# Kernel optimization log

Hardware: AMD Instinct MI355X
Metric: run time of the kernel (lower is better)

Reference implementation:

```python
import jax, jax.numpy as jnp
import numpy as np
import math

B, T, Z, H, DOF = 256, 200, 64, 256, 12
NUM_LINKS = 13
POS_DIM = (NUM_LINKS + 1) * 3  # 42
TIME_BANDS = 6
TIME_DIM = 2 * TIME_BANDS + 1  # 13
ACTION_SCALE = 0.25
TRACK_ALPHA = 1.0
SIGMA_MIN, SIGMA_MAX = 0.05, 0.5


def setup_inputs() -> dict:
    key = jax.random.key(0)
    ks = iter(jax.random.split(key, 32))
    rn = lambda shape, s=0.1: jax.random.normal(next(ks), shape, jnp.float32) * s
    inp = {
        'z': jax.random.normal(next(ks), (B, Z), jnp.float32),
        'W_hz': rn((H, Z)), 'b_hz': rn((H,)),
        'W_cz': rn((H, Z)), 'b_cz': rn((H,)),
        'Wih': rn((4 * H, DOF + Z + TIME_DIM)), 'Whh': rn((4 * H, H)),
        'bih': rn((4 * H,)), 'bhh': rn((4 * H,)),
        'Wp1': rn((H, H)), 'bp1': rn((H,)),
        'Wp2': rn((DOF, H)), 'bp2': rn((DOF,)),
        'Wo1': rn((H, H)), 'bo1': rn((H,)),
        'Wo2': rn((3, H)), 'bo2': rn((3,)),
        'Wv': rn((POS_DIM, H)), 'bv': rn((POS_DIM,)),
        'Wfk': rn((NUM_LINKS * 3, DOF)), 'bfk': rn((NUM_LINKS * 3,)),
        'pos_mean': jax.random.normal(next(ks), (NUM_LINKS + 1, 3), jnp.float32),
        'pos_std': 0.5 + jax.random.uniform(next(ks), (NUM_LINKS + 1, 3), jnp.float32),
        'joint_lower': -jnp.ones((DOF,), jnp.float32),
        'joint_upper': jnp.ones((DOF,), jnp.float32),
        'default_dof_pos': jnp.zeros((DOF,), jnp.float32),
    }
    return inp


def _time_features():
    t = jnp.linspace(0.0, 1.0, T)
    feats = [t]
    for k in range(TIME_BANDS):
        f = 2.0 ** k
        feats.append(jnp.sin(2 * math.pi * f * t))
        feats.append(jnp.cos(2 * math.pi * f * t))
    return jnp.stack(feats, axis=-1)  # [T, TIME_DIM]


def reference(z, W_hz, b_hz, W_cz, b_cz, Wih, Whh, bih, bhh,
              Wp1, bp1, Wp2, bp2, Wo1, bo1, Wo2, bo2, Wv, bv, Wfk, bfk,
              pos_mean, pos_std, joint_lower, joint_upper, default_dof_pos):
    joint_range = (joint_upper - joint_lower) / 2.0
    joint_mean = (joint_upper + joint_lower) / 2.0
    time_feats = _time_features()  # [T, TIME_DIM]

    h0 = z @ W_hz.T + b_hz  # [B,H]
    c0 = z @ W_cz.T + b_cz
    prev0 = jnp.broadcast_to(default_dof_pos, (B, DOF))

    def step(carry, tf):
        h, c, prev = carry
        prev_norm = (prev - joint_mean) / joint_range
        x = jnp.concatenate([prev_norm, z, jnp.broadcast_to(tf, (B, TIME_DIM))], axis=-1)
        g = x @ Wih.T + bih + h @ Whh.T + bhh  # [B,4H]
        i, f, gg, o = jnp.split(g, 4, axis=-1)
        c_new = jax.nn.sigmoid(f) * c + jax.nn.sigmoid(i) * jnp.tanh(gg)
        h_new = jax.nn.sigmoid(o) * jnp.tanh(c_new)
        action = jnp.tanh(jax.nn.relu(h_new @ Wp1.T + bp1) @ Wp2.T + bp2)
        target = action * ACTION_SCALE + default_dof_pos
        cur = prev + TRACK_ALPHA * (target - prev)
        clamped = jnp.clip(cur, joint_lower, joint_upper)
        cur_in = cur + jax.lax.stop_gradient(clamped - cur)  # straight-through clamp
        obj = jax.nn.relu(h_new @ Wo1.T + bo1) @ Wo2.T + bo2
        return (h_new, c_new, jax.lax.stop_gradient(cur_in)), (h_new, action, cur, obj)

    _, (H_seq, actions, joints, objs) = jax.lax.scan(step, (h0, c0, prev0), time_feats)
    # [T,B,*] -> [B,T,*]
    H_seq = jnp.swapaxes(H_seq, 0, 1)
    actions_seq = jnp.swapaxes(actions, 0, 1)
    joint_traj = jnp.swapaxes(joints, 0, 1)
    object_traj = jnp.swapaxes(objs, 0, 1)

    agent_traj = joint_traj @ Wfk.T + bfk  # FK: [B,T,39]
    combined = jnp.concatenate([agent_traj, object_traj], axis=-1)  # [B,T,42]
    combined_rs = combined.reshape(B, T, NUM_LINKS + 1, 3)
    graph_x_mu = ((combined_rs - pos_mean) / pos_std).reshape(B, T, POS_DIM)

    sigma = SIGMA_MIN + (SIGMA_MAX - SIGMA_MIN) * jax.nn.sigmoid(H_seq @ Wv.T + bv)
    log_sigma_pos = jnp.log(sigma)
    return (graph_x_mu, joint_traj, actions_seq, log_sigma_pos)
```

## Files before the change

### kernel.cpp

```cpp
#include <hip/hip_runtime.h>
#include <math.h>

#define B_ 256
#define T_ 200
#define H_ 256
#define DOF_ 12

typedef __bf16 bf16;
typedef __bf16 bf16x8 __attribute__((ext_vector_type(8)));
typedef float f32x4 __attribute__((ext_vector_type(4)));
typedef unsigned long long u64;

#define XK 288
#define XPAD 296
#define P1PAD 264

#define PI_D 3.14159265358979323846

#define OFF_TF     0u
#define OFF_TCONP  10400u
#define OFF_ZCP    829600u
#define OFF_H0     1878176u
#define OFF_C0     2140320u
#define OFF_WCOMB  2402464u
#define OFF_WP1    2992288u
#define OFF_WP2    3123360u
#define OFF_WO1    3131552u
#define OFF_WO2    3262624u
#define OFF_WV     3270816u
#define OFF_HX     3295392u
#define OFF_HSEQ   3819680u

__device__ __forceinline__ float sigf(float x) { return 1.f / (1.f + __expf(-x)); }
__device__ __forceinline__ float tanh_f(float x) {
  float a = fabsf(x);
  float e = __expf(-2.f * a);
  float t = (1.f - e) / (1.f + e);
  return x < 0.f ? -t : t;
}

#define LBAR() asm volatile("s_waitcnt lgkmcnt(0)\n\ts_barrier" ::: "memory")

__global__ void k_tfeat(float* tf) {
  int i = blockIdx.x * blockDim.x + threadIdx.x;
  if (i >= T_ * 13) return;
  int t = i / 13, j = i % 13;
  float tv = (float)t / 199.f;
  float v;
  if (j == 0) v = tv;
  else {
    int k = (j - 1) >> 1;
    float f = (float)(1 << k);
    double arg = 2.0 * PI_D * (double)f * (double)tv;
    v = (j & 1) ? (float)sin(arg) : (float)cos(arg);
  }
  tf[i] = v;
}

__global__ void k_prep(const float* __restrict__ tf, const float* __restrict__ Wih,
                       const float* __restrict__ z,
                       const float* __restrict__ bih, const float* __restrict__ bhh,
                       const float* __restrict__ Whz, const float* __restrict__ bhz,
                       const float* __restrict__ Wcz, const float* __restrict__ bcz,
                       float* tconp, float* zcp, float* h0, float* c0) {
  int i = blockIdx.x * blockDim.x + threadIdx.x;
  if (i < 204800) {
    int g = i & 3, q = i >> 2;
    int m = q & 127, hm = (q >> 7) & 1, t = q >> 8;
    int n = g * 256 + 128 * hm + m;
    float s = 0.f;
    #pragma unroll
    for (int j = 0; j < 13; ++j) s += tf[t * 13 + j] * Wih[n * 89 + 76 + j];
    tconp[i] = s;
    return;
  }
  i -= 204800;
  if (i < 262144) {
    int r = i & 3, g = (i >> 2) & 3, tid = (i >> 4) & 511;
    int half = (i >> 13) & 1, pairk = i >> 14;
    int wv = tid >> 6, lr = tid & 15, lq = (tid >> 4) & 3;
    int b = pairk * 16 + lq * 4 + r;
    int n = g * 256 + 128 * half + 16 * wv + lr;
    float s = bih[n] + bhh[n];
    for (int k = 0; k < 64; ++k) s += z[b * 64 + k] * Wih[n * 89 + 12 + k];
    zcp[i] = s;
    return;
  }
  i -= 262144;
  if (i < 65536) {
    int b = i / 256, u = i % 256;
    float s = bhz[u];
    for (int k = 0; k < 64; ++k) s += z[b * 64 + k] * Whz[u * 64 + k];
    h0[i] = s;
    return;
  }
  i -= 65536;
  if (i < 65536) {
    int b = i / 256, u = i % 256;
    float s = bcz[u];
    for (int k = 0; k < 64; ++k) s += z[b * 64 + k] * Wcz[u * 64 + k];
    c0[i] = s;
  }
}

__global__ void k_cast(const float* __restrict__ Whh, const float* __restrict__ Wih,
                       const float* __restrict__ Wp1, const float* __restrict__ Wp2,
                       const float* __restrict__ Wo1, const float* __restrict__ Wo2,
                       const float* __restrict__ Wv,
                       bf16* Wcomb, bf16* Wp1b, bf16* Wp2b, bf16* Wo1b,
                       bf16* Wo2b, bf16* Wvb) {
  int i = blockIdx.x * blockDim.x + threadIdx.x;
  if (i < 294912) {
    int n = i / XK, k = i % XK;
    float v = (k < 256) ? Whh[n * 256 + k]
            : ((k < 268) ? Wih[n * 89 + (k - 256)] : 0.f);
    Wcomb[i] = (bf16)v;
    return;
  }
  i -= 294912;
  if (i < 65536) { Wp1b[i] = (bf16)Wp1[i]; return; }
  i -= 65536;
  if (i < 4096) { int r = i / 256; Wp2b[i] = (bf16)((r < 12) ? Wp2[i] : 0.f); return; }
  i -= 4096;
  if (i < 65536) { Wo1b[i] = (bf16)Wo1[i]; return; }
  i -= 65536;
  if (i < 4096) { int r = i / 256; Wo2b[i] = (bf16)((r < 3) ? Wo2[i] : 0.f); return; }
  i -= 4096;
  if (i < 12288) { int r = i / 256; Wvb[i] = (bf16)((r < 42) ? Wv[i] : 0.f); }
}

__global__ __launch_bounds__(512, 2) void k_recur(
    const float* __restrict__ zcp, const float* __restrict__ tconp,
    const float* __restrict__ h0, const float* __restrict__ c0,
    const bf16* __restrict__ Wcomb, const bf16* __restrict__ Wp1b,
    const bf16* __restrict__ Wp2b,
    const float* __restrict__ bp1, const float* __restrict__ bp2,
    const float* __restrict__ jlo, const float* __restrict__ jhi,
    const float* __restrict__ ddp,
    u64* hxt,
    bf16* __restrict__ Hseq, float* __restrict__ outJ, float* __restrict__ outA) {
  __shared__ bf16 xbuf[16][XPAD];
  __shared__ bf16 w1[272][P1PAD];
  __shared__ bf16 p1buf[16][P1PAD];
  const int tid = threadIdx.x;
  const int wv = tid >> 6, ln = tid & 63, lr = ln & 15, lq = ln >> 4;
  const int bid = blockIdx.x;
  const int pairk = ((bid >> 4) << 3) | (bid & 7);
  const int half = (bid >> 3) & 1;
  const int lbid = pairk * 2 + half;
  const int b0 = pairk * 16;
  const int u_loc = 16 * wv + lr;
  const int u_gl = 128 * half + u_loc;

  for (int i = tid; i < 272 * 32; i += 512) {
    int r = i >> 5, c8 = (i & 31) * 8;
    bf16x8 v = (r < 256)
      ? *reinterpret_cast<const bf16x8*>(&Wp1b[r * 256 + c8])
      : *reinterpret_cast<const bf16x8*>(&Wp2b[(r - 256) * 256 + c8]);
    *reinterpret_cast<bf16x8*>(&w1[r][c8]) = v;
  }
  for (int i = tid; i < 16 * XPAD; i += 512) {
    int r = i / XPAD, c = i % XPAD;
    float v = 0.f;
    if (c < 256) v = h0[(b0 + r) * 256 + c];
    else if (c < 268) {
      int d = c - 256;
      float lo = jlo[d], hi = jhi[d];
      v = (ddp[d] - 0.5f * (hi + lo)) / (0.5f * (hi - lo));
    }
    xbuf[r][c] = (bf16)v;
  }

  f32x4 wc0[9], wc1[9], wc2[9], wc3[9];
  #pragma unroll
  for (int kt = 0; kt < 9; ++kt) {
    wc0[kt] = *reinterpret_cast<const f32x4*>(&Wcomb[(size_t)(0 * 256 + u_gl) * XK + kt * 32 + lq * 8]);
    wc1[kt] = *reinterpret_cast<const f32x4*>(&Wcomb[(size_t)(1 * 256 + u_gl) * XK + kt * 32 + lq * 8]);
    wc2[kt] = *reinterpret_cast<const f32x4*>(&Wcomb[(size_t)(2 * 256 + u_gl) * XK + kt * 32 + lq * 8]);
    wc3[kt] = *reinterpret_cast<const f32x4*>(&Wcomb[(size_t)(3 * 256 + u_gl) * XK + kt * 32 + lq * 8]);
    asm volatile("" : "+a"(wc0[kt]), "+a"(wc1[kt]), "+a"(wc2[kt]), "+a"(wc3[kt]));
  }

  float c_reg[4];
  #pragma unroll
  for (int r = 0; r < 4; ++r) c_reg[r] = c0[(b0 + lq * 4 + r) * 256 + u_gl];
  f32x4 zcreg[4];
  #pragma unroll
  for (int g = 0; g < 4; ++g)
    zcreg[g] = *reinterpret_cast<const f32x4*>(
        zcp + ((size_t)lbid * 512 + tid) * 16 + g * 4);
  const float* tcb = tconp + (size_t)(half * 512 + u_loc * 4);
  const float bp1r0 = bp1[32 * wv + lr];
  const float bp1r1 = bp1[32 * wv + 16 + lr];
  float bp2r = 0.f, ddr = 0.f, lor = -1.f, hir = 1.f;
  if (lr < 12) { bp2r = bp2[lr]; ddr = ddp[lr]; lor = jlo[lr]; hir = jhi[lr]; }
  const float jmr = 0.5f * (hir + lor), jrr = 0.5f * (hir - lor);
  bf16* hs = Hseq + ((size_t)(b0 + lq * 4) * T_) * 256 + u_gl;

  const int wru = 16 * wv + (ln >> 2), wrc = ln & 3;
  const int rcol = 128 * (half ^ 1) + wru;
  u64* pws0 = hxt + ((((size_t)(pairk * 2 + 0) * 2 + half) * 128 + u_loc) * 4 + lq) * 2;
  u64* pws1 = hxt + ((((size_t)(pairk * 2 + 1) * 2 + half) * 128 + u_loc) * 4 + lq) * 2;
  u64* prs0 = hxt + ((((size_t)(pairk * 2 + 0) * 2 + (half ^ 1)) * 128 + wru) * 4 + wrc) * 2;
  u64* prs1 = hxt + ((((size_t)(pairk * 2 + 1) * 2 + (half ^ 1)) * 128 + wru) * 4 + wrc) * 2;

  f32x4 tcv = *reinterpret_cast<const f32x4*>(tcb);
  __syncthreads();
  bool dead = false;

  for (int t = 0; t < T_; ++t) {
    f32x4 ac[4];
    #pragma unroll
    for (int g = 0; g < 4; ++g) ac[g] = zcreg[g] + tcv[g];
    #pragma unroll
    for (int kt = 0; kt < 9; ++kt) {
      bf16x8 a = *reinterpret_cast<const bf16x8*>(&xbuf[lr][kt * 32 + lq * 8]);
      asm volatile("" : "+a"(wc0[kt]), "+a"(wc1[kt]), "+a"(wc2[kt]), "+a"(wc3[kt]));
      ac[0] = __builtin_amdgcn_mfma_f32_16x16x32_bf16(a, __builtin_bit_cast(bf16x8, wc0[kt]), ac[0], 0, 0, 0);
      ac[1] = __builtin_amdgcn_mfma_f32_16x16x32_bf16(a, __builtin_bit_cast(bf16x8, wc1[kt]), ac[1], 0, 0, 0);
      ac[2] = __builtin_amdgcn_mfma_f32_16x16x32_bf16(a, __builtin_bit_cast(bf16x8, wc2[kt]), ac[2], 0, 0, 0);
      ac[3] = __builtin_amdgcn_mfma_f32_16x16x32_bf16(a, __builtin_bit_cast(bf16x8, wc3[kt]), ac[3], 0, 0, 0);
    }
    LBAR();

    union { u64 v[1]; unsigned short s[4]; } pk;
    bf16 hb4[4];
    #pragma unroll
    for (int r = 0; r < 4; ++r) {
      float cn = sigf(ac[1][r]) * c_reg[r] + sigf(ac[0][r]) * tanh_f(ac[2][r]);
      float hn = sigf(ac[3][r]) * tanh_f(cn);
      c_reg[r] = cn;
      bf16 hb = (bf16)hn;
      hb4[r] = hb;
      pk.s[r] = __builtin_bit_cast(unsigned short, hb);
    }
    const unsigned int want = t + 1;
    {
      u64 q0 = ((u64)want << 32) | (u64)pk.s[0] | ((u64)pk.s[1] << 16);
      u64 q1 = ((u64)want << 32) | (u64)pk.s[2] | ((u64)pk.s[3] << 16);
      u64* pw = (t & 1) ? pws1 : pws0;
      __hip_atomic_store(pw, q0, __ATOMIC_RELAXED, __HIP_MEMORY_SCOPE_AGENT);
      __hip_atomic_store(pw + 1, q1, __ATOMIC_RELAXED, __HIP_MEMORY_SCOPE_AGENT);
    }
    #pragma unroll
    for (int r = 0; r < 4; ++r) {
      xbuf[lq * 4 + r][u_gl] = hb4[r];
      hs[(size_t)r * (T_ * 256) + (size_t)t * 256] = hb4[r];
    }
    f32x4 tcn = *reinterpret_cast<const f32x4*>(
        tcb + (size_t)((t + 1 < T_) ? t + 1 : t) * 1024);

    u64 pq0, pq1;
    {
      u64* pr = (t & 1) ? prs1 : prs0;
      int guard = 1 << 16;
      for (;;) {
        pq0 = __hip_atomic_load(pr, __ATOMIC_RELAXED, __HIP_MEMORY_SCOPE_AGENT);
        pq1 = __hip_atomic_load(pr + 1, __ATOMIC_RELAXED, __HIP_MEMORY_SCOPE_AGENT);
        int ok = ((unsigned)(pq0 >> 32) == want) & ((unsigned)(pq1 >> 32) == want);
        if (__all(ok)) break;
        if (dead || --guard == 0) { dead = true; break; }
      }
    }
    xbuf[wrc * 4 + 0][rcol] = __builtin_bit_cast(bf16, (unsigned short)(pq0));
    xbuf[wrc * 4 + 1][rcol] = __builtin_bit_cast(bf16, (unsigned short)(pq0 >> 16));
    xbuf[wrc * 4 + 2][rcol] = __builtin_bit_cast(bf16, (unsigned short)(pq1));
    xbuf[wrc * 4 + 3][rcol] = __builtin_bit_cast(bf16, (unsigned short)(pq1 >> 16));
    LBAR();

    {
      f32x4 acc0 = {bp1r0, bp1r0, bp1r0, bp1r0};
      f32x4 acc1 = {bp1r1, bp1r1, bp1r1, bp1r1};
      #pragma unroll
      for (int kt = 0; kt < 8; ++kt) {
        bf16x8 av = *reinterpret_cast<const bf16x8*>(&xbuf[lr][kt * 32 + lq * 8]);
        bf16x8 b0v = *reinterpret_cast<const bf16x8*>(&w1[32 * wv + lr][kt * 32 + lq * 8]);
        bf16x8 b1v = *reinterpret_cast<const bf16x8*>(&w1[32 * wv + 16 + lr][kt * 32 + lq * 8]);
        acc0 = __builtin_amdgcn_mfma_f32_16x16x32_bf16(av, b0v, acc0, 0, 0, 0);
        acc1 = __builtin_amdgcn_mfma_f32_16x16x32_bf16(av, b1v, acc1, 0, 0, 0);
      }
      #pragma unroll
      for (int r = 0; r < 4; ++r) {
        p1buf[lq * 4 + r][32 * wv + lr] = (bf16)fmaxf(acc0[r], 0.f);
        p1buf[lq * 4 + r][32 * wv + 16 + lr] = (bf16)fmaxf(acc1[r], 0.f);
      }
    }
    LBAR();

    if (wv == 0) {
      f32x4 acc = {0.f, 0.f, 0.f, 0.f};
      #pragma unroll
      for (int kt = 0; kt < 8; ++kt) {
        bf16x8 ap = *reinterpret_cast<const bf16x8*>(&p1buf[lr][kt * 32 + lq * 8]);
        bf16x8 w2 = *reinterpret_cast<const bf16x8*>(&w1[256 + lr][kt * 32 + lq * 8]);
        acc = __builtin_amdgcn_mfma_f32_16x16x32_bf16(ap, w2, acc, 0, 0, 0);
      }
      if (lr < 12) {
        #pragma unroll
        for (int r = 0; r < 4; ++r) {
          int b = lq * 4 + r;
          float act = tanh_f(acc[r] + bp2r);
          float curp = act * 0.25f + ddr;
          float cl = fminf(fmaxf(curp, lor), hir);
          if (half == 0) {
            size_t o = ((size_t)(b0 + b) * T_ + t) * 12 + lr;
            outA[o] = act;
            outJ[o] = curp;
          }
          xbuf[b][256 + lr] = (bf16)((cl - jmr) / jrr);
        }
      }
    }
    LBAR();
    tcv = tcn;
  }
}

__global__ __launch_bounds__(256) void k_post(
    const bf16* __restrict__ Hseq, const bf16* __restrict__ Wo1b,
    const bf16* __restrict__ Wo2b, const bf16* __restrict__ Wvb,
    const float* __restrict__ bo1, const float* __restrict__ bo2,
    const float* __restrict__ bv,
    const float* __restrict__ Wfk, const float* __restrict__ bfk,
    const float* __restrict__ pm, const float* __restrict__ ps,
    const float* __restrict__ joints, float* __restrict__ out0,
    float* __restrict__ out3) {
  __shared__ bf16 u1buf[16][P1PAD];
  __shared__ float objbuf[16][3];
  __shared__ float jbuf[16][12];
  const int tid = threadIdx.x;
  const int wv = tid >> 6;
  const int ln = tid & 63;
  const int lr = ln & 15;
  const int lq = ln >> 4;

  bf16x8 wo1f[4][8];
  float bo1r[4];
  #pragma unroll
  for (int jn = 0; jn < 4; ++jn) {
    int n0 = wv * 64 + jn * 16;
    bo1r[jn] = bo1[n0 + lr];
    #pragma unroll
    for (int kt = 0; kt < 8; ++kt)
      wo1f[jn][kt] = *reinterpret_cast<const bf16x8*>(
          &Wo1b[(size_t)(n0 + lr) * 256 + kt * 32 + lq * 8]);
  }
  const int col = (wv - 1) * 16 + lr;
  bf16x8 wvf[8];
  float bvr = 0.f;
  if (wv >= 1) {
    #pragma unroll
    for (int kt = 0; kt < 8; ++kt)
      wvf[kt] = *reinterpret_cast<const bf16x8*>(
          &Wvb[(size_t)col * 256 + kt * 32 + lq * 8]);
    bvr = (col < 42) ? bv[col] : 0.f;
  }
  bf16x8 wo2f[8];
  if (wv == 0) {
    #pragma unroll
    for (int kt = 0; kt < 8; ++kt)
      wo2f[kt] = *reinterpret_cast<const bf16x8*>(
          &Wo2b[(size_t)lr * 256 + kt * 32 + lq * 8]);
  }

  for (int it = 0; it < 10; ++it) {
    int tt = blockIdx.x * 10 + it;
    size_t r0 = (size_t)tt * 16;
    bf16x8 ah[8];
    #pragma unroll
    for (int kt = 0; kt < 8; ++kt)
      ah[kt] = *reinterpret_cast<const bf16x8*>(&Hseq[(r0 + lr) * 256 + kt * 32 + lq * 8]);
    #pragma unroll
    for (int jn = 0; jn < 4; ++jn) {
      int n0 = wv * 64 + jn * 16;
      float bb = bo1r[jn];
      f32x4 acc = {bb, bb, bb, bb};
      #pragma unroll
      for (int kt = 0; kt < 8; ++kt)
        acc = __builtin_amdgcn_mfma_f32_16x16x32_bf16(ah[kt], wo1f[jn][kt], acc, 0, 0, 0);
      #pragma unroll
      for (int r = 0; r < 4; ++r)
        u1buf[lq * 4 + r][n0 + lr] = (bf16)fmaxf(acc[r], 0.f);
    }
    if (wv >= 1) {
      f32x4 acc = {bvr, bvr, bvr, bvr};
      #pragma unroll
      for (int kt = 0; kt < 8; ++kt)
        acc = __builtin_amdgcn_mfma_f32_16x16x32_bf16(ah[kt], wvf[kt], acc, 0, 0, 0);
      if (col < 42) {
        #pragma unroll
        for (int r = 0; r < 4; ++r) {
          float s = 0.05f + 0.45f * sigf(acc[r]);
          out3[(r0 + lq * 4 + r) * 42 + col] = __logf(s);
        }
      }
    }
    if (tid < 192) {
      int rr = tid / 12, d = tid % 12;
      jbuf[rr][d] = joints[(r0 + rr) * 12 + d];
    }
    __syncthreads();
    if (wv == 0) {
      bf16x8 ap[8];
      #pragma unroll
      for (int kt = 0; kt < 8; ++kt)
        ap[kt] = *reinterpret_cast<const bf16x8*>(&u1buf[lr][kt * 32 + lq * 8]);
      f32x4 acc = {0.f, 0.f, 0.f, 0.f};
      #pragma unroll
      for (int kt = 0; kt < 8; ++kt)
        acc = __builtin_amdgcn_mfma_f32_16x16x32_bf16(ap[kt], wo2f[kt], acc, 0, 0, 0);
      if (lr < 3) {
        #pragma unroll
        for (int r = 0; r < 4; ++r)
          objbuf[lq * 4 + r][lr] = acc[r] + bo2[lr];
      }
    }
    __syncthreads();
    for (int e = tid; e < 16 * 42; e += 256) {
      int rr = e / 42, pd = e % 42;
      float v;
      if (pd < 39) {
        float s = bfk[pd];
        #pragma unroll
        for (int d = 0; d < 12; ++d) s += jbuf[rr][d] * Wfk[pd * 12 + d];
        v = s;
      } else v = objbuf[rr][pd - 39];
      out0[(r0 + rr) * 42 + pd] = (v - pm[pd]) / ps[pd];
    }
    __syncthreads();
  }
}

extern "C" void kernel_launch(void* const* d_in, const int* in_sizes, int n_in,
                              void* d_out, int out_size, void* d_ws, size_t ws_size,
                              hipStream_t stream) {
  const float* z   = (const float*)d_in[0];
  const float* Whz = (const float*)d_in[1];
  const float* bhz = (const float*)d_in[2];
  const float* Wcz = (const float*)d_in[3];
  const float* bcz = (const float*)d_in[4];
  const float* Wih = (const float*)d_in[5];
  const float* Whh = (const float*)d_in[6];
  const float* bih = (const float*)d_in[7];
  const float* bhh = (const float*)d_in[8];
  const float* Wp1 = (const float*)d_in[9];
  const float* bp1 = (const float*)d_in[10];
  const float* Wp2 = (const float*)d_in[11];
  const float* bp2 = (const float*)d_in[12];
  const float* Wo1 = (const float*)d_in[13];
  const float* bo1 = (const float*)d_in[14];
  const float* Wo2 = (const float*)d_in[15];
  const float* bo2 = (const float*)d_in[16];
  const float* Wv  = (const float*)d_in[17];
  const float* bv  = (const float*)d_in[18];
  const float* Wfk = (const float*)d_in[19];
  const float* bfk = (const float*)d_in[20];
  const float* pm  = (const float*)d_in[21];
  const float* ps  = (const float*)d_in[22];
  const float* jlo = (const float*)d_in[23];
  const float* jhi = (const float*)d_in[24];
  const float* ddp = (const float*)d_in[25];

  char* ws = (char*)d_ws;
  float* tf    = (float*)(ws + OFF_TF);
  float* tconp = (float*)(ws + OFF_TCONP);
  float* zcp   = (float*)(ws + OFF_ZCP);
  float* h0    = (float*)(ws + OFF_H0);
  float* c0    = (float*)(ws + OFF_C0);
  bf16* Wcomb  = (bf16*)(ws + OFF_WCOMB);
  bf16* Wp1b   = (bf16*)(ws + OFF_WP1);
  bf16* Wp2b   = (bf16*)(ws + OFF_WP2);
  bf16* Wo1b   = (bf16*)(ws + OFF_WO1);
  bf16* Wo2b   = (bf16*)(ws + OFF_WO2);
  bf16* Wvb    = (bf16*)(ws + OFF_WV);
  u64* hxt     = (u64*)(ws + OFF_HX);
  bf16* Hseq   = (bf16*)(ws + OFF_HSEQ);

  float* out  = (float*)d_out;
  float* out0 = out;
  float* outJ = out + 2150400;
  float* outA = out + 2764800;
  float* out3 = out + 3379200;

  k_tfeat<<<11, 256, 0, stream>>>(tf);
  k_prep<<<2336, 256, 0, stream>>>(tf, Wih, z, bih, bhh, Whz, bhz, Wcz, bcz,
                                   tconp, zcp, h0, c0);
  k_cast<<<1744, 256, 0, stream>>>(Whh, Wih, Wp1, Wp2, Wo1, Wo2, Wv,
                                   Wcomb, Wp1b, Wp2b, Wo1b, Wo2b, Wvb);
  k_recur<<<32, 512, 0, stream>>>(zcp, tconp, h0, c0, Wcomb, Wp1b, Wp2b,
                                  bp1, bp2, jlo, jhi, ddp, hxt,
                                  Hseq, outJ, outA);
  k_post<<<320, 256, 0, stream>>>(Hseq, Wo1b, Wo2b, Wvb, bo1, bo2, bv,
                                  Wfk, bfk, pm, ps, outJ, out0, out3);
}
```

Measured before the change: 1.119 ms.

## Halve recurrent kernel block size, giving each wave two hidden-unit tiles

The recurrent LSTM kernel now runs 256 threads (4 waves) per block instead of 512, and each wave computes two 16-unit slices of the gate GEMM, keeping twice as many weight fragments in accumulation registers. The cross-block hidden-state exchange reads four packed words per lane instead of two, and the Wp1 stage issues four MFMAs per k-step per wave. The intent is cheaper per-step barriers and more MFMA work per wave on the serial critical path, at the cost of register pressure (72 AGPR vectors) and less latency hiding. tanh also uses a hardware reciprocal instead of a divide.

```diff
diff --git a/kernel.cpp b/kernel.cpp
--- a/kernel.cpp
+++ b/kernel.cpp
@@ -35,7 +35,7 @@
 __device__ __forceinline__ float tanh_f(float x) {
   float a = fabsf(x);
   float e = __expf(-2.f * a);
-  float t = (1.f - e) / (1.f + e);
+  float t = (1.f - e) * __builtin_amdgcn_rcpf(1.f + e);
   return x < 0.f ? -t : t;
 }
 
@@ -129,7 +129,7 @@
   if (i < 12288) { int r = i / 256; Wvb[i] = (bf16)((r < 42) ? Wv[i] : 0.f); }
 }
 
-__global__ __launch_bounds__(512, 2) void k_recur(
+__global__ __launch_bounds__(256, 1) void k_recur(
     const float* __restrict__ zcp, const float* __restrict__ tconp,
     const float* __restrict__ h0, const float* __restrict__ c0,
     const bf16* __restrict__ Wcomb, const bf16* __restrict__ Wp1b,
@@ -149,17 +149,15 @@
   const int half = (bid >> 3) & 1;
   const int lbid = pairk * 2 + half;
   const int b0 = pairk * 16;
-  const int u_loc = 16 * wv + lr;
-  const int u_gl = 128 * half + u_loc;
-
-  for (int i = tid; i < 272 * 32; i += 512) {
+
+  for (int i = tid; i < 272 * 32; i += 256) {
     int r = i >> 5, c8 = (i & 31) * 8;
     bf16x8 v = (r < 256)
       ? *reinterpret_cast<const bf16x8*>(&Wp1b[r * 256 + c8])
       : *reinterpret_cast<const bf16x8*>(&Wp2b[(r - 256) * 256 + c8]);
     *reinterpret_cast<bf16x8*>(&w1[r][c8]) = v;
   }
-  for (int i = tid; i < 16 * XPAD; i += 512) {
+  for (int i = tid; i < 16 * XPAD; i += 256) {
     int r = i / XPAD, c = i % XPAD;
     float v = 0.f;
     if (c < 256) v = h0[(b0 + r) * 256 + c];
@@ -171,118 +169,173 @@
     xbuf[r][c] = (bf16)v;
   }
 
-  f32x4 wc0[9], wc1[9], wc2[9], wc3[9];
-  #pragma unroll
-  for (int kt = 0; kt < 9; ++kt) {
-    wc0[kt] = *reinterpret_cast<const f32x4*>(&Wcomb[(size_t)(0 * 256 + u_gl) * XK + kt * 32 + lq * 8]);
-    wc1[kt] = *reinterpret_cast<const f32x4*>(&Wcomb[(size_t)(1 * 256 + u_gl) * XK + kt * 32 + lq * 8]);
-    wc2[kt] = *reinterpret_cast<const f32x4*>(&Wcomb[(size_t)(2 * 256 + u_gl) * XK + kt * 32 + lq * 8]);
-    wc3[kt] = *reinterpret_cast<const f32x4*>(&Wcomb[(size_t)(3 * 256 + u_gl) * XK + kt * 32 + lq * 8]);
-    asm volatile("" : "+a"(wc0[kt]), "+a"(wc1[kt]), "+a"(wc2[kt]), "+a"(wc3[kt]));
-  }
-
-  float c_reg[4];
-  #pragma unroll
-  for (int r = 0; r < 4; ++r) c_reg[r] = c0[(b0 + lq * 4 + r) * 256 + u_gl];
-  f32x4 zcreg[4];
-  #pragma unroll
-  for (int g = 0; g < 4; ++g)
-    zcreg[g] = *reinterpret_cast<const f32x4*>(
-        zcp + ((size_t)lbid * 512 + tid) * 16 + g * 4);
-  const float* tcb = tconp + (size_t)(half * 512 + u_loc * 4);
-  const float bp1r0 = bp1[32 * wv + lr];
-  const float bp1r1 = bp1[32 * wv + 16 + lr];
+  f32x4 wc[2][4][9];
+  #pragma unroll
+  for (int ji = 0; ji < 2; ++ji) {
+    const int ug = 128 * half + 32 * wv + 16 * ji + lr;
+    #pragma unroll
+    for (int g = 0; g < 4; ++g)
+      #pragma unroll
+      for (int kt = 0; kt < 9; ++kt)
+        wc[ji][g][kt] = *reinterpret_cast<const f32x4*>(
+            &Wcomb[(size_t)(g * 256 + ug) * XK + kt * 32 + lq * 8]);
+  }
+  #pragma unroll
+  for (int kt = 0; kt < 9; ++kt)
+    asm volatile("" : "+a"(wc[0][0][kt]), "+a"(wc[0][1][kt]),
+                      "+a"(wc[0][2][kt]), "+a"(wc[0][3][kt]),
+                      "+a"(wc[1][0][kt]), "+a"(wc[1][1][kt]),
+                      "+a"(wc[1][2][kt]), "+a"(wc[1][3][kt]));
+
+  float c_reg[2][4];
+  f32x4 zcreg[2][4];
+  bf16* hs[2];
+  #pragma unroll
+  for (int ji = 0; ji < 2; ++ji) {
+    const int ug = 128 * half + 32 * wv + 16 * ji + lr;
+    #pragma unroll
+    for (int r = 0; r < 4; ++r) c_reg[ji][r] = c0[(b0 + lq * 4 + r) * 256 + ug];
+    const int tid512 = (2 * wv + ji) * 64 + ln;
+    #pragma unroll
+    for (int g = 0; g < 4; ++g)
+      zcreg[ji][g] = *reinterpret_cast<const f32x4*>(
+          zcp + ((size_t)lbid * 512 + tid512) * 16 + g * 4);
+    hs[ji] = Hseq + ((size_t)(b0 + lq * 4) * T_) * 256 + ug;
+  }
+  const float* tcb0 = tconp + (size_t)(half * 512 + (32 * wv + lr) * 4);
+  const float* tcb1 = tcb0 + 64;
+  float bp1r[4];
+  #pragma unroll
+  for (int jn = 0; jn < 4; ++jn) bp1r[jn] = bp1[64 * wv + 16 * jn + lr];
   float bp2r = 0.f, ddr = 0.f, lor = -1.f, hir = 1.f;
   if (lr < 12) { bp2r = bp2[lr]; ddr = ddp[lr]; lor = jlo[lr]; hir = jhi[lr]; }
   const float jmr = 0.5f * (hir + lor), jrr = 0.5f * (hir - lor);
-  bf16* hs = Hseq + ((size_t)(b0 + lq * 4) * T_) * 256 + u_gl;
-
-  const int wru = 16 * wv + (ln >> 2), wrc = ln & 3;
-  const int rcol = 128 * (half ^ 1) + wru;
-  u64* pws0 = hxt + ((((size_t)(pairk * 2 + 0) * 2 + half) * 128 + u_loc) * 4 + lq) * 2;
-  u64* pws1 = hxt + ((((size_t)(pairk * 2 + 1) * 2 + half) * 128 + u_loc) * 4 + lq) * 2;
-  u64* prs0 = hxt + ((((size_t)(pairk * 2 + 0) * 2 + (half ^ 1)) * 128 + wru) * 4 + wrc) * 2;
-  u64* prs1 = hxt + ((((size_t)(pairk * 2 + 1) * 2 + (half ^ 1)) * 128 + wru) * 4 + wrc) * 2;
-
-  f32x4 tcv = *reinterpret_cast<const f32x4*>(tcb);
+
+  u64* pws[2][2];
+  #pragma unroll
+  for (int ji = 0; ji < 2; ++ji) {
+    const int ul = 32 * wv + 16 * ji + lr;
+    #pragma unroll
+    for (int s = 0; s < 2; ++s)
+      pws[ji][s] = hxt + ((((size_t)(pairk * 2 + s) * 2 + half) * 128 + ul) * 4 + lq) * 2;
+  }
+  const int ru = 32 * wv + (ln >> 1);
+  const int rcol = 128 * (half ^ 1) + ru;
+  const int row0 = (ln & 1) * 8;
+  u64* prs[2];
+  #pragma unroll
+  for (int s = 0; s < 2; ++s)
+    prs[s] = hxt + ((((size_t)(pairk * 2 + s) * 2 + (half ^ 1)) * 128 + ru) * 4 + 2 * (ln & 1)) * 2;
+
+  f32x4 tcv0 = *reinterpret_cast<const f32x4*>(tcb0);
+  f32x4 tcv1 = *reinterpret_cast<const f32x4*>(tcb1);
   __syncthreads();
   bool dead = false;
 
   for (int t = 0; t < T_; ++t) {
-    f32x4 ac[4];
-    #pragma unroll
-    for (int g = 0; g < 4; ++g) ac[g] = zcreg[g] + tcv[g];
+    f32x4 ac[2][4];
+    #pragma unroll
+    for (int g = 0; g < 4; ++g) { ac[0][g] = zcreg[0][g] + tcv0[g]; ac[1][g] = zcreg[1][g] + tcv1[g]; }
     #pragma unroll
     for (int kt = 0; kt < 9; ++kt) {
       bf16x8 a = *reinterpret_cast<const bf16x8*>(&xbuf[lr][kt * 32 + lq * 8]);
-      asm volatile("" : "+a"(wc0[kt]), "+a"(wc1[kt]), "+a"(wc2[kt]), "+a"(wc3[kt]));
-      ac[0] = __builtin_amdgcn_mfma_f32_16x16x32_bf16(a, __builtin_bit_cast(bf16x8, wc0[kt]), ac[0], 0, 0, 0);
-      ac[1] = __builtin_amdgcn_mfma_f32_16x16x32_bf16(a, __builtin_bit_cast(bf16x8, wc1[kt]), ac[1], 0, 0, 0);
-      ac[2] = __builtin_amdgcn_mfma_f32_16x16x32_bf16(a, __builtin_bit_cast(bf16x8, wc2[kt]), ac[2], 0, 0, 0);
-      ac[3] = __builtin_amdgcn_mfma_f32_16x16x32_bf16(a, __builtin_bit_cast(bf16x8, wc3[kt]), ac[3], 0, 0, 0);
+      asm volatile("" : "+a"(wc[0][0][kt]), "+a"(wc[0][1][kt]),
+                        "+a"(wc[0][2][kt]), "+a"(wc[0][3][kt]),
+                        "+a"(wc[1][0][kt]), "+a"(wc[1][1][kt]),
+                        "+a"(wc[1][2][kt]), "+a"(wc[1][3][kt]));
+      #pragma unroll
+      for (int ji = 0; ji < 2; ++ji)
+        #pragma unroll
+        for (int g = 0; g < 4; ++g)
+          ac[ji][g] = __builtin_amdgcn_mfma_f32_16x16x32_bf16(
+              a, __builtin_bit_cast(bf16x8, wc[ji][g][kt]), ac[ji][g], 0, 0, 0);
     }
     LBAR();
 
-    union { u64 v[1]; unsigned short s[4]; } pk;
-    bf16 hb4[4];
-    #pragma unroll
-    for (int r = 0; r < 4; ++r) {
-      float cn = sigf(ac[1][r]) * c_reg[r] + sigf(ac[0][r]) * tanh_f(ac[2][r]);
-      float hn = sigf(ac[3][r]) * tanh_f(cn);
-      c_reg[r] = cn;
-      bf16 hb = (bf16)hn;
-      hb4[r] = hb;
-      pk.s[r] = __builtin_bit_cast(unsigned short, hb);
-    }
     const unsigned int want = t + 1;
-    {
-      u64 q0 = ((u64)want << 32) | (u64)pk.s[0] | ((u64)pk.s[1] << 16);
-      u64 q1 = ((u64)want << 32) | (u64)pk.s[2] | ((u64)pk.s[3] << 16);
-      u64* pw = (t & 1) ? pws1 : pws0;
+    bf16 hb[2][4];
+    #pragma unroll
+    for (int ji = 0; ji < 2; ++ji) {
+      unsigned short s4[4];
+      #pragma unroll
+      for (int r = 0; r < 4; ++r) {
+        float cn = sigf(ac[ji][1][r]) * c_reg[ji][r] + sigf(ac[ji][0][r]) * tanh_f(ac[ji][2][r]);
+        float hn = sigf(ac[ji][3][r]) * tanh_f(cn);
+        c_reg[ji][r] = cn;
+        bf16 h = (bf16)hn;
+        hb[ji][r] = h;
+        s4[r] = __builtin_bit_cast(unsigned short, h);
+      }
+      u64 q0 = ((u64)want << 32) | (u64)s4[0] | ((u64)s4[1] << 16);
+      u64 q1 = ((u64)want << 32) | (u64)s4[2] | ((u64)s4[3] << 16);
+      u64* pw = pws[ji][t & 1];
       __hip_atomic_store(pw, q0, __ATOMIC_RELAXED, __HIP_MEMORY_SCOPE_AGENT);
       __hip_atomic_store(pw + 1, q1, __ATOMIC_RELAXED, __HIP_MEMORY_SCOPE_AGENT);
     }
     #pragma unroll
-    for (int r = 0; r < 4; ++r) {
-      xbuf[lq * 4 + r][u_gl] = hb4[r];
-      hs[(size_t)r * (T_ * 256) + (size_t)t * 256] = hb4[r];
-    }
-    f32x4 tcn = *reinterpret_cast<const f32x4*>(
-        tcb + (size_t)((t + 1 < T_) ? t + 1 : t) * 1024);
-
-    u64 pq0, pq1;
+    for (int ji = 0; ji < 2; ++ji) {
+      const int ug = 128 * half + 32 * wv + 16 * ji + lr;
+      #pragma unroll
+      for (int r = 0; r < 4; ++r) {
+        xbuf[lq * 4 + r][ug] = hb[ji][r];
+        hs[ji][(size_t)r * (T_ * 256) + (size_t)t * 256] = hb[ji][r];
+      }
+    }
     {
-      u64* pr = (t & 1) ? prs1 : prs0;
+      size_t tp = (size_t)((t + 1 < T_) ? t + 1 : t) * 1024;
+      f32x4 tn0 = *reinterpret_cast<const f32x4*>(tcb0 + tp);
+      f32x4 tn1 = *reinterpret_cast<const f32x4*>(tcb1 + tp);
+      tcv0 = tn0; tcv1 = tn1;
+    }
+
+    u64 pq0, pq1, pq2, pq3;
+    {
+      u64* pr = prs[t & 1];
       int guard = 1 << 16;
       for (;;) {
-        pq0 = __hip_atomic_load(pr, __ATOMIC_RELAXED, __HIP_MEMORY_SCOPE_AGENT);
+        pq0 = __hip_atomic_load(pr + 0, __ATOMIC_RELAXED, __HIP_MEMORY_SCOPE_AGENT);
         pq1 = __hip_atomic_load(pr + 1, __ATOMIC_RELAXED, __HIP_MEMORY_SCOPE_AGENT);
-        int ok = ((unsigned)(pq0 >> 32) == want) & ((unsigned)(pq1 >> 32) == want);
+        pq2 = __hip_atomic_load(pr + 2, __ATOMIC_RELAXED, __HIP_MEMORY_SCOPE_AGENT);
+        pq3 = __hip_atomic_load(pr + 3, __ATOMIC_RELAXED, __HIP_MEMORY_SCOPE_AGENT);
+        int ok = ((unsigned)(pq0 >> 32) == want) & ((unsigned)(pq1 >> 32) == want) &
+                 ((unsigned)(pq2 >> 32) == want) & ((unsigned)(pq3 >> 32) == want);
         if (__all(ok)) break;
         if (dead || --guard == 0) { dead = true; break; }
       }
     }
-    xbuf[wrc * 4 + 0][rcol] = __builtin_bit_cast(bf16, (unsigned short)(pq0));
-    xbuf[wrc * 4 + 1][rcol] = __builtin_bit_cast(bf16, (unsigned short)(pq0 >> 16));
-    xbuf[wrc * 4 + 2][rcol] = __builtin_bit_cast(bf16, (unsigned short)(pq1));
-    xbuf[wrc * 4 + 3][rcol] = __builtin_bit_cast(bf16, (unsigned short)(pq1 >> 16));
+    xbuf[row0 + 0][rcol] = __builtin_bit_cast(bf16, (unsigned short)(pq0));
+    xbuf[row0 + 1][rcol] = __builtin_bit_cast(bf16, (unsigned short)(pq0 >> 16));
+    xbuf[row0 + 2][rcol] = __builtin_bit_cast(bf16, (unsigned short)(pq1));
+    xbuf[row0 + 3][rcol] = __builtin_bit_cast(bf16, (unsigned short)(pq1 >> 16));
+    xbuf[row0 + 4][rcol] = __builtin_bit_cast(bf16, (unsigned short)(pq2));
+    xbuf[row0 + 5][rcol] = __builtin_bit_cast(bf16, (unsigned short)(pq2 >> 16));
+    xbuf[row0 + 6][rcol] = __builtin_bit_cast(bf16, (unsigned short)(pq3));
+    xbuf[row0 + 7][rcol] = __builtin_bit_cast(bf16, (unsigned short)(pq3 >> 16));
     LBAR();
 
     {
-      f32x4 acc0 = {bp1r0, bp1r0, bp1r0, bp1r0};
-      f32x4 acc1 = {bp1r1, bp1r1, bp1r1, bp1r1};
+      f32x4 pa0 = {bp1r[0], bp1r[0], bp1r[0], bp1r[0]};
+      f32x4 pa1 = {bp1r[1], bp1r[1], bp1r[1], bp1r[1]};
+      f32x4 pa2 = {bp1r[2], bp1r[2], bp1r[2], bp1r[2]};
+      f32x4 pa3 = {bp1r[3], bp1r[3], bp1r[3], bp1r[3]};
       #pragma unroll
       for (int kt = 0; kt < 8; ++kt) {
         bf16x8 av = *reinterpret_cast<const bf16x8*>(&xbuf[lr][kt * 32 + lq * 8]);
-        bf16x8 b0v = *reinterpret_cast<const bf16x8*>(&w1[32 * wv + lr][kt * 32 + lq * 8]);
-        bf16x8 b1v = *reinterpret_cast<const bf16x8*>(&w1[32 * wv + 16 + lr][kt * 32 + lq * 8]);
-        acc0 = __builtin_amdgcn_mfma_f32_16x16x32_bf16(av, b0v, acc0, 0, 0, 0);
-        acc1 = __builtin_amdgcn_mfma_f32_16x16x32_bf16(av, b1v, acc1, 0, 0, 0);
+        bf16x8 b0v = *reinterpret_cast<const bf16x8*>(&w1[64 * wv + lr][kt * 32 + lq * 8]);
+        bf16x8 b1v = *reinterpret_cast<const bf16x8*>(&w1[64 * wv + 16 + lr][kt * 32 + lq * 8]);
+        bf16x8 b2v = *reinterpret_cast<const bf16x8*>(&w1[64 * wv + 32 + lr][kt * 32 + lq * 8]);
+        bf16x8 b3v = *reinterpret_cast<const bf16x8*>(&w1[64 * wv + 48 + lr][kt * 32 + lq * 8]);
+        pa0 = __builtin_amdgcn_mfma_f32_16x16x32_bf16(av, b0v, pa0, 0, 0, 0);
+        pa1 = __builtin_amdgcn_mfma_f32_16x16x32_bf16(av, b1v, pa1, 0, 0, 0);
+        pa2 = __builtin_amdgcn_mfma_f32_16x16x32_bf16(av, b2v, pa2, 0, 0, 0);
+        pa3 = __builtin_amdgcn_mfma_f32_16x16x32_bf16(av, b3v, pa3, 0, 0, 0);
       }
       #pragma unroll
       for (int r = 0; r < 4; ++r) {
-        p1buf[lq * 4 + r][32 * wv + lr] = (bf16)fmaxf(acc0[r], 0.f);
-        p1buf[lq * 4 + r][32 * wv + 16 + lr] = (bf16)fmaxf(acc1[r], 0.f);
+        p1buf[lq * 4 + r][64 * wv + lr]      = (bf16)fmaxf(pa0[r], 0.f);
+        p1buf[lq * 4 + r][64 * wv + 16 + lr] = (bf16)fmaxf(pa1[r], 0.f);
+        p1buf[lq * 4 + r][64 * wv + 32 + lr] = (bf16)fmaxf(pa2[r], 0.f);
+        p1buf[lq * 4 + r][64 * wv + 48 + lr] = (bf16)fmaxf(pa3[r], 0.f);
       }
     }
     LBAR();
@@ -312,7 +365,6 @@
       }
     }
     LBAR();
-    tcv = tcn;
   }
 }
 
@@ -487,7 +539,7 @@
                                    tconp, zcp, h0, c0);
   k_cast<<<1744, 256, 0, stream>>>(Whh, Wih, Wp1, Wp2, Wo1, Wo2, Wv,
                                    Wcomb, Wp1b, Wp2b, Wo1b, Wo2b, Wvb);
-  k_recur<<<32, 512, 0, stream>>>(zcp, tconp, h0, c0, Wcomb, Wp1b, Wp2b,
+  k_recur<<<32, 256, 0, stream>>>(zcp, tconp, h0, c0, Wcomb, Wp1b, Wp2b,
                                   bp1, bp2, jlo, jhi, ddp, hxt,
                                   Hseq, outJ, outA);
   k_post<<<320, 256, 0, stream>>>(Hseq, Wo1b, Wo2b, Wvb, bo1, bo2, bv,
```

Measured after the change: 1.102 ms. About the same (-1.5%).

## Split LSTM recurrence hidden units across four blocks per batch group

Applied to the files above, without the earlier changes.

The recurrent kernel now splits each 16-row batch group's hidden units over four 256-thread blocks instead of two 512-thread blocks. That gives 64 blocks, each exchanging h slices with three peers through flag-tagged global atomics. Each wave now does a quarter of the hidden units, and the zc and time-bias terms are loaded from global memory every step instead of being held in registers. The aim is more parallelism across CUs on the serial time loop, at the cost of more cross-block polling traffic and sync latency per step; tanh division is also replaced by a hardware reciprocal.

```diff
diff --git a/kernel.cpp b/kernel.cpp
--- a/kernel.cpp
+++ b/kernel.cpp
@@ -35,7 +35,7 @@
 __device__ __forceinline__ float tanh_f(float x) {
   float a = fabsf(x);
   float e = __expf(-2.f * a);
-  float t = (1.f - e) / (1.f + e);
+  float t = (1.f - e) * __builtin_amdgcn_rcpf(1.f + e);
   return x < 0.f ? -t : t;
 }
 
@@ -65,9 +65,8 @@
                        float* tconp, float* zcp, float* h0, float* c0) {
   int i = blockIdx.x * blockDim.x + threadIdx.x;
   if (i < 204800) {
-    int g = i & 3, q = i >> 2;
-    int m = q & 127, hm = (q >> 7) & 1, t = q >> 8;
-    int n = g * 256 + 128 * hm + m;
+    int g = i & 3, u = (i >> 2) & 255, t = i >> 10;
+    int n = g * 256 + u;
     float s = 0.f;
     #pragma unroll
     for (int j = 0; j < 13; ++j) s += tf[t * 13 + j] * Wih[n * 89 + 76 + j];
@@ -76,11 +75,11 @@
   }
   i -= 204800;
   if (i < 262144) {
-    int r = i & 3, g = (i >> 2) & 3, tid = (i >> 4) & 511;
-    int half = (i >> 13) & 1, pairk = i >> 14;
-    int wv = tid >> 6, lr = tid & 15, lq = (tid >> 4) & 3;
-    int b = pairk * 16 + lq * 4 + r;
-    int n = g * 256 + 128 * half + 16 * wv + lr;
+    int r = i & 3, g = (i >> 2) & 3, tid = (i >> 4) & 255, bid = i >> 12;
+    int quarter = bid >> 4, grp = bid & 15;
+    int wv = tid >> 6, ln = tid & 63, lr = ln & 15, lq = (ln >> 4) & 3;
+    int b = grp * 16 + lq * 4 + r;
+    int n = g * 256 + 64 * quarter + 16 * wv + lr;
     float s = bih[n] + bhh[n];
     for (int k = 0; k < 64; ++k) s += z[b * 64 + k] * Wih[n * 89 + 12 + k];
     zcp[i] = s;
@@ -129,7 +128,7 @@
   if (i < 12288) { int r = i / 256; Wvb[i] = (bf16)((r < 42) ? Wv[i] : 0.f); }
 }
 
-__global__ __launch_bounds__(512, 2) void k_recur(
+__global__ __launch_bounds__(256, 1) void k_recur(
     const float* __restrict__ zcp, const float* __restrict__ tconp,
     const float* __restrict__ h0, const float* __restrict__ c0,
     const bf16* __restrict__ Wcomb, const bf16* __restrict__ Wp1b,
@@ -145,21 +144,18 @@
   const int tid = threadIdx.x;
   const int wv = tid >> 6, ln = tid & 63, lr = ln & 15, lq = ln >> 4;
   const int bid = blockIdx.x;
-  const int pairk = ((bid >> 4) << 3) | (bid & 7);
-  const int half = (bid >> 3) & 1;
-  const int lbid = pairk * 2 + half;
-  const int b0 = pairk * 16;
-  const int u_loc = 16 * wv + lr;
-  const int u_gl = 128 * half + u_loc;
-
-  for (int i = tid; i < 272 * 32; i += 512) {
+  const int quarter = bid >> 4, grp = bid & 15;
+  const int b0 = grp * 16;
+  const int u_gl = 64 * quarter + 16 * wv + lr;
+
+  for (int i = tid; i < 272 * 32; i += 256) {
     int r = i >> 5, c8 = (i & 31) * 8;
     bf16x8 v = (r < 256)
       ? *reinterpret_cast<const bf16x8*>(&Wp1b[r * 256 + c8])
       : *reinterpret_cast<const bf16x8*>(&Wp2b[(r - 256) * 256 + c8]);
     *reinterpret_cast<bf16x8*>(&w1[r][c8]) = v;
   }
-  for (int i = tid; i < 16 * XPAD; i += 512) {
+  for (int i = tid; i < 16 * XPAD; i += 256) {
     int r = i / XPAD, c = i % XPAD;
     float v = 0.f;
     if (c < 256) v = h0[(b0 + r) * 256 + c];
@@ -171,119 +167,148 @@
     xbuf[r][c] = (bf16)v;
   }
 
-  f32x4 wc0[9], wc1[9], wc2[9], wc3[9];
+  f32x4 wc[4][9];
   #pragma unroll
-  for (int kt = 0; kt < 9; ++kt) {
-    wc0[kt] = *reinterpret_cast<const f32x4*>(&Wcomb[(size_t)(0 * 256 + u_gl) * XK + kt * 32 + lq * 8]);
-    wc1[kt] = *reinterpret_cast<const f32x4*>(&Wcomb[(size_t)(1 * 256 + u_gl) * XK + kt * 32 + lq * 8]);
-    wc2[kt] = *reinterpret_cast<const f32x4*>(&Wcomb[(size_t)(2 * 256 + u_gl) * XK + kt * 32 + lq * 8]);
-    wc3[kt] = *reinterpret_cast<const f32x4*>(&Wcomb[(size_t)(3 * 256 + u_gl) * XK + kt * 32 + lq * 8]);
-    asm volatile("" : "+a"(wc0[kt]), "+a"(wc1[kt]), "+a"(wc2[kt]), "+a"(wc3[kt]));
-  }
+  for (int g = 0; g < 4; ++g)
+    #pragma unroll
+    for (int kt = 0; kt < 9; ++kt)
+      wc[g][kt] = *reinterpret_cast<const f32x4*>(
+          &Wcomb[(size_t)(g * 256 + u_gl) * XK + kt * 32 + lq * 8]);
+  #pragma unroll
+  for (int kt = 0; kt < 9; ++kt)
+    asm volatile("" : "+a"(wc[0][kt]), "+a"(wc[1][kt]),
+                      "+a"(wc[2][kt]), "+a"(wc[3][kt]));
 
   float c_reg[4];
   #pragma unroll
   for (int r = 0; r < 4; ++r) c_reg[r] = c0[(b0 + lq * 4 + r) * 256 + u_gl];
-  f32x4 zcreg[4];
+  const int zc_i = (bid * 256 + tid) * 16;
+  int tc_i = u_gl * 4;
+  int hs_i = ((b0 + lq * 4) * T_) * 256 + u_gl;
+  const int pw_i = (grp * 8 + quarter) * 512 + (16 * wv + lr) * 8 + lq * 2;
+  const int ru = tid >> 2, rlq = tid & 3;
+  const int rrow0 = rlq * 4;
+  const int q1 = (quarter + 1) & 3, q2 = (quarter + 2) & 3, q3 = (quarter + 3) & 3;
+  const int pr1 = (grp * 8 + q1) * 512 + ru * 8 + rlq * 2;
+  const int pr2 = (grp * 8 + q2) * 512 + ru * 8 + rlq * 2;
+  const int pr3 = (grp * 8 + q3) * 512 + ru * 8 + rlq * 2;
+
+  float bp1r[4];
   #pragma unroll
-  for (int g = 0; g < 4; ++g)
-    zcreg[g] = *reinterpret_cast<const f32x4*>(
-        zcp + ((size_t)lbid * 512 + tid) * 16 + g * 4);
-  const float* tcb = tconp + (size_t)(half * 512 + u_loc * 4);
-  const float bp1r0 = bp1[32 * wv + lr];
-  const float bp1r1 = bp1[32 * wv + 16 + lr];
+  for (int jn = 0; jn < 4; ++jn) bp1r[jn] = bp1[64 * wv + 16 * jn + lr];
   float bp2r = 0.f, ddr = 0.f, lor = -1.f, hir = 1.f;
   if (lr < 12) { bp2r = bp2[lr]; ddr = ddp[lr]; lor = jlo[lr]; hir = jhi[lr]; }
   const float jmr = 0.5f * (hir + lor), jrr = 0.5f * (hir - lor);
-  bf16* hs = Hseq + ((size_t)(b0 + lq * 4) * T_) * 256 + u_gl;
-
-  const int wru = 16 * wv + (ln >> 2), wrc = ln & 3;
-  const int rcol = 128 * (half ^ 1) + wru;
-  u64* pws0 = hxt + ((((size_t)(pairk * 2 + 0) * 2 + half) * 128 + u_loc) * 4 + lq) * 2;
-  u64* pws1 = hxt + ((((size_t)(pairk * 2 + 1) * 2 + half) * 128 + u_loc) * 4 + lq) * 2;
-  u64* prs0 = hxt + ((((size_t)(pairk * 2 + 0) * 2 + (half ^ 1)) * 128 + wru) * 4 + wrc) * 2;
-  u64* prs1 = hxt + ((((size_t)(pairk * 2 + 1) * 2 + (half ^ 1)) * 128 + wru) * 4 + wrc) * 2;
-
-  f32x4 tcv = *reinterpret_cast<const f32x4*>(tcb);
+
   __syncthreads();
   bool dead = false;
 
   for (int t = 0; t < T_; ++t) {
+    f32x4 zc[4], tcv;
+    #pragma unroll
+    for (int g = 0; g < 4; ++g)
+      zc[g] = *reinterpret_cast<const f32x4*>(zcp + zc_i + g * 4);
+    tcv = *reinterpret_cast<const f32x4*>(tconp + tc_i);
+    tc_i += 1024;
+
     f32x4 ac[4];
     #pragma unroll
-    for (int g = 0; g < 4; ++g) ac[g] = zcreg[g] + tcv[g];
+    for (int g = 0; g < 4; ++g) ac[g] = (f32x4){0.f, 0.f, 0.f, 0.f};
     #pragma unroll
     for (int kt = 0; kt < 9; ++kt) {
       bf16x8 a = *reinterpret_cast<const bf16x8*>(&xbuf[lr][kt * 32 + lq * 8]);
-      asm volatile("" : "+a"(wc0[kt]), "+a"(wc1[kt]), "+a"(wc2[kt]), "+a"(wc3[kt]));
-      ac[0] = __builtin_amdgcn_mfma_f32_16x16x32_bf16(a, __builtin_bit_cast(bf16x8, wc0[kt]), ac[0], 0, 0, 0);
-      ac[1] = __builtin_amdgcn_mfma_f32_16x16x32_bf16(a, __builtin_bit_cast(bf16x8, wc1[kt]), ac[1], 0, 0, 0);
-      ac[2] = __builtin_amdgcn_mfma_f32_16x16x32_bf16(a, __builtin_bit_cast(bf16x8, wc2[kt]), ac[2], 0, 0, 0);
-      ac[3] = __builtin_amdgcn_mfma_f32_16x16x32_bf16(a, __builtin_bit_cast(bf16x8, wc3[kt]), ac[3], 0, 0, 0);
-    }
+      asm volatile("" : "+a"(wc[0][kt]), "+a"(wc[1][kt]),
+                        "+a"(wc[2][kt]), "+a"(wc[3][kt]));
+      #pragma unroll
+      for (int g = 0; g < 4; ++g)
+        ac[g] = __builtin_amdgcn_mfma_f32_16x16x32_bf16(
+            a, __builtin_bit_cast(bf16x8, wc[g][kt]), ac[g], 0, 0, 0);
+    }
+    #pragma unroll
+    for (int g = 0; g < 4; ++g) ac[g] += zc[g] + tcv[g];
     LBAR();
 
-    union { u64 v[1]; unsigned short s[4]; } pk;
-    bf16 hb4[4];
+    const unsigned int want = t + 1;
+    bf16 hb[4];
+    unsigned short s4[4];
     #pragma unroll
     for (int r = 0; r < 4; ++r) {
       float cn = sigf(ac[1][r]) * c_reg[r] + sigf(ac[0][r]) * tanh_f(ac[2][r]);
       float hn = sigf(ac[3][r]) * tanh_f(cn);
       c_reg[r] = cn;
-      bf16 hb = (bf16)hn;
-      hb4[r] = hb;
-      pk.s[r] = __builtin_bit_cast(unsigned short, hb);
-    }
-    const unsigned int want = t + 1;
+      bf16 h = (bf16)hn;
+      hb[r] = h;
+      s4[r] = __builtin_bit_cast(unsigned short, h);
+    }
     {
-      u64 q0 = ((u64)want << 32) | (u64)pk.s[0] | ((u64)pk.s[1] << 16);
-      u64 q1 = ((u64)want << 32) | (u64)pk.s[2] | ((u64)pk.s[3] << 16);
-      u64* pw = (t & 1) ? pws1 : pws0;
-      __hip_atomic_store(pw, q0, __ATOMIC_RELAXED, __HIP_MEMORY_SCOPE_AGENT);
-      __hip_atomic_store(pw + 1, q1, __ATOMIC_RELAXED, __HIP_MEMORY_SCOPE_AGENT);
+      u64 q0 = ((u64)want << 32) | (u64)s4[0] | ((u64)s4[1] << 16);
+      u64 qq1 = ((u64)want << 32) | (u64)s4[2] | ((u64)s4[3] << 16);
+      int pwi = pw_i + (t & 1) * 2048;
+      __hip_atomic_store(hxt + pwi, q0, __ATOMIC_RELAXED, __HIP_MEMORY_SCOPE_AGENT);
+      __hip_atomic_store(hxt + pwi + 1, qq1, __ATOMIC_RELAXED, __HIP_MEMORY_SCOPE_AGENT);
     }
     #pragma unroll
     for (int r = 0; r < 4; ++r) {
-      xbuf[lq * 4 + r][u_gl] = hb4[r];
-      hs[(size_t)r * (T_ * 256) + (size_t)t * 256] = hb4[r];
-    }
-    f32x4 tcn = *reinterpret_cast<const f32x4*>(
-        tcb + (size_t)((t + 1 < T_) ? t + 1 : t) * 1024);
-
-    u64 pq0, pq1;
+      xbuf[lq * 4 + r][u_gl] = hb[r];
+      Hseq[hs_i + r * (T_ * 256)] = hb[r];
+    }
+    hs_i += 256;
+
+    u64 pa0, pa1, pb0, pb1, pc0, pc1;
     {
-      u64* pr = (t & 1) ? prs1 : prs0;
+      const int so = (t & 1) * 2048;
       int guard = 1 << 16;
       for (;;) {
-        pq0 = __hip_atomic_load(pr, __ATOMIC_RELAXED, __HIP_MEMORY_SCOPE_AGENT);
-        pq1 = __hip_atomic_load(pr + 1, __ATOMIC_RELAXED, __HIP_MEMORY_SCOPE_AGENT);
-        int ok = ((unsigned)(pq0 >> 32) == want) & ((unsigned)(pq1 >> 32) == want);
+        pa0 = __hip_atomic_load(hxt + pr1 + so, __ATOMIC_RELAXED, __HIP_MEMORY_SCOPE_AGENT);
+        pa1 = __hip_atomic_load(hxt + pr1 + so + 1, __ATOMIC_RELAXED, __HIP_MEMORY_SCOPE_AGENT);
+        pb0 = __hip_atomic_load(hxt + pr2 + so, __ATOMIC_RELAXED, __HIP_MEMORY_SCOPE_AGENT);
+        pb1 = __hip_atomic_load(hxt + pr2 + so + 1, __ATOMIC_RELAXED, __HIP_MEMORY_SCOPE_AGENT);
+        pc0 = __hip_atomic_load(hxt + pr3 + so, __ATOMIC_RELAXED, __HIP_MEMORY_SCOPE_AGENT);
+        pc1 = __hip_atomic_load(hxt + pr3 + so + 1, __ATOMIC_RELAXED, __HIP_MEMORY_SCOPE_AGENT);
+        int ok = ((unsigned)(pa0 >> 32) == want) & ((unsigned)(pa1 >> 32) == want) &
+                 ((unsigned)(pb0 >> 32) == want) & ((unsigned)(pb1 >> 32) == want) &
+                 ((unsigned)(pc0 >> 32) == want) & ((unsigned)(pc1 >> 32) == want);
         if (__all(ok)) break;
         if (dead || --guard == 0) { dead = true; break; }
       }
     }
-    xbuf[wrc * 4 + 0][rcol] = __builtin_bit_cast(bf16, (unsigned short)(pq0));
-    xbuf[wrc * 4 + 1][rcol] = __builtin_bit_cast(bf16, (unsigned short)(pq0 >> 16));
-    xbuf[wrc * 4 + 2][rcol] = __builtin_bit_cast(bf16, (unsigned short)(pq1));
-    xbuf[wrc * 4 + 3][rcol] = __builtin_bit_cast(bf16, (unsigned short)(pq1 >> 16));
+    {
+      int col1 = 64 * q1 + ru, col2 = 64 * q2 + ru, col3 = 64 * q3 + ru;
+      xbuf[rrow0 + 0][col1] = __builtin_bit_cast(bf16, (unsigned short)(pa0));
+      xbuf[rrow0 + 1][col1] = __builtin_bit_cast(bf16, (unsigned short)(pa0 >> 16));
+      xbuf[rrow0 + 2][col1] = __builtin_bit_cast(bf16, (unsigned short)(pa1));
+      xbuf[rrow0 + 3][col1] = __builtin_bit_cast(bf16, (unsigned short)(pa1 >> 16));
+      xbuf[rrow0 + 0][col2] = __builtin_bit_cast(bf16, (unsigned short)(pb0));
+      xbuf[rrow0 + 1][col2] = __builtin_bit_cast(bf16, (unsigned short)(pb0 >> 16));
+      xbuf[rrow0 + 2][col2] = __builtin_bit_cast(bf16, (unsigned short)(pb1));
+      xbuf[rrow0 + 3][col2] = __builtin_bit_cast(bf16, (unsigned short)(pb1 >> 16));
+      xbuf[rrow0 + 0][col3] = __builtin_bit_cast(bf16, (unsigned short)(pc0));
+      xbuf[rrow0 + 1][col3] = __builtin_bit_cast(bf16, (unsigned short)(pc0 >> 16));
+      xbuf[rrow0 + 2][col3] = __builtin_bit_cast(bf16, (unsigned short)(pc1));
+      xbuf[rrow0 + 3][col3] = __builtin_bit_cast(bf16, (unsigned short)(pc1 >> 16));
+    }
     LBAR();
 
     {
-      f32x4 acc0 = {bp1r0, bp1r0, bp1r0, bp1r0};
-      f32x4 acc1 = {bp1r1, bp1r1, bp1r1, bp1r1};
+      f32x4 pa[4];
+      #pragma unroll
+      for (int jn = 0; jn < 4; ++jn)
+        pa[jn] = (f32x4){bp1r[jn], bp1r[jn], bp1r[jn], bp1r[jn]};
       #pragma unroll
       for (int kt = 0; kt < 8; ++kt) {
         bf16x8 av = *reinterpret_cast<const bf16x8*>(&xbuf[lr][kt * 32 + lq * 8]);
-        bf16x8 b0v = *reinterpret_cast<const bf16x8*>(&w1[32 * wv + lr][kt * 32 + lq * 8]);
-        bf16x8 b1v = *reinterpret_cast<const bf16x8*>(&w1[32 * wv + 16 + lr][kt * 32 + lq * 8]);
-        acc0 = __builtin_amdgcn_mfma_f32_16x16x32_bf16(av, b0v, acc0, 0, 0, 0);
-        acc1 = __builtin_amdgcn_mfma_f32_16x16x32_bf16(av, b1v, acc1, 0, 0, 0);
+        #pragma unroll
+        for (int jn = 0; jn < 4; ++jn) {
+          bf16x8 bv = *reinterpret_cast<const bf16x8*>(
+              &w1[64 * wv + 16 * jn + lr][kt * 32 + lq * 8]);
+          pa[jn] = __builtin_amdgcn_mfma_f32_16x16x32_bf16(av, bv, pa[jn], 0, 0, 0);
+        }
       }
       #pragma unroll
-      for (int r = 0; r < 4; ++r) {
-        p1buf[lq * 4 + r][32 * wv + lr] = (bf16)fmaxf(acc0[r], 0.f);
-        p1buf[lq * 4 + r][32 * wv + 16 + lr] = (bf16)fmaxf(acc1[r], 0.f);
-      }
+      for (int jn = 0; jn < 4; ++jn)
+        #pragma unroll
+        for (int r = 0; r < 4; ++r)
+          p1buf[lq * 4 + r][64 * wv + 16 * jn + lr] = (bf16)fmaxf(pa[jn][r], 0.f);
     }
     LBAR();
 
@@ -302,7 +327,7 @@
           float act = tanh_f(acc[r] + bp2r);
           float curp = act * 0.25f + ddr;
           float cl = fminf(fmaxf(curp, lor), hir);
-          if (half == 0) {
+          if (quarter == 0) {
             size_t o = ((size_t)(b0 + b) * T_ + t) * 12 + lr;
             outA[o] = act;
             outJ[o] = curp;
@@ -312,7 +337,6 @@
       }
     }
     LBAR();
-    tcv = tcn;
   }
 }
 
@@ -487,7 +511,7 @@
                                    tconp, zcp, h0, c0);
   k_cast<<<1744, 256, 0, stream>>>(Whh, Wih, Wp1, Wp2, Wo1, Wo2, Wv,
                                    Wcomb, Wp1b, Wp2b, Wo1b, Wo2b, Wvb);
-  k_recur<<<32, 512, 0, stream>>>(zcp, tconp, h0, c0, Wcomb, Wp1b, Wp2b,
+  k_recur<<<64, 256, 0, stream>>>(zcp, tconp, h0, c0, Wcomb, Wp1b, Wp2b,
                                   bp1, bp2, jlo, jhi, ddp, hxt,
                                   Hseq, outJ, outA);
   k_post<<<320, 256, 0, stream>>>(Hseq, Wo1b, Wo2b, Wvb, bo1, bo2, bv,
```

After: 965.7 us. 1.16x faster.
